# Performance work log

Hardware: AMD Instinct MI355X
Metric: run time of the kernel (lower is better)

## Reference

```python
import jax, jax.numpy as jnp
import numpy as np

SCALE = 256 ** -0.5  # d_proj ** -0.5

def setup_inputs() -> dict:
    key = jax.random.key(0)
    k1, k2, k3, k4 = jax.random.split(key, 4)
    B, L, T = 8, 2048, 512
    Dh, Dg, Dp = 1024, 768, 256
    H = jax.random.normal(k1, (B, L, Dh), dtype=jnp.float32)
    G = jax.random.normal(k2, (B, T, Dg), dtype=jnp.float32)
    mask = jnp.zeros((B, L), dtype=jnp.int32)  # True/nonzero = masked OUT
    Wk = jax.random.normal(k3, (Dh, Dp), dtype=jnp.float32) * (Dh ** -0.5)
    Wq = jax.random.normal(k4, (Dg, Dp), dtype=jnp.float32) * (Dg ** -0.5)
    return {"H": H, "G": G, "mask": mask, "Wk": Wk, "Wq": Wq}

def reference(H, G, mask, Wk, Wq):
    # K: [B,L,Dp], Q: [B,T,Dp]
    K = jnp.einsum('bld,dp->blp', H, Wk)
    Q = jnp.einsum('btd,dp->btp', G, Wq)
    # logits over keys L: [B,T,L]
    logits = jnp.einsum('btp,blp->btl', Q, K) * SCALE
    logits = jnp.where(mask[:, None, :] != 0, -jnp.inf, logits)
    alpha = jax.nn.softmax(logits, axis=-1)  # online-softmax in torch == exact softmax
    Z = jnp.einsum('btl,bld->btd', alpha, H)  # [B,T,Dh]
    return Z
```

## Files before the change

### kernel.cpp

```cpp
#include <hip/hip_runtime.h>
#include <math.h>

#define BATCH 8
#define LKEYS 2048
#define TQ    512
#define DH    1024
#define DG    768
#define DP    256
#define SCALE 0.0625f

typedef short  short8  __attribute__((ext_vector_type(8)));
typedef float  floatx4 __attribute__((ext_vector_type(4)));
typedef unsigned short u16x4 __attribute__((ext_vector_type(4)));
typedef unsigned short u16x8 __attribute__((ext_vector_type(8)));

typedef unsigned int __attribute__((address_space(1))) as1_uint;
typedef unsigned int __attribute__((address_space(3))) as3_uint;

__device__ __forceinline__ unsigned short f2b(float f) {
    union { float f; unsigned int u; } v; v.f = f;
    unsigned int u = v.u;
    unsigned int r = u + 0x7fffu + ((u >> 16) & 1u);
    if ((u & 0x7f800000u) == 0x7f800000u) r = u;
    return (unsigned short)(r >> 16);
}

__device__ __forceinline__ void gload_lds16(const void* g, void* l) {
    __builtin_amdgcn_global_load_lds((const as1_uint*)g, (as3_uint*)l, 16, 0, 0);
}

__host__ __device__ constexpr int wcnt_vm(int vm) {
    return (vm & 15) | (7 << 4) | (15 << 8);
}

template<int BM, int BN, int OMODE, int SWZ, int KSPLIT>
__global__ __launch_bounds__(256) void gemm_bf16_p(
    const unsigned short* __restrict__ Ap, const unsigned short* __restrict__ Bp,
    const int* __restrict__ maskp, void* __restrict__ Cp,
    int K, int lda, int ldb, int ldc,
    long sA, long sB, long sC, long sM, long sP, float scale)
{
    constexpr int FM = BM / 32, FN = BN / 32;
    constexpr int AI = BM / 64, BI = BN / 64;
    constexpr int NL = AI + BI;

    __shared__ unsigned short As[4][BM * 32];
    __shared__ unsigned short Bs[4][BN * 32];

    int bx = blockIdx.x, by = blockIdx.y, zz = blockIdx.z;
    if (SWZ == 1) {
        const int gx = gridDim.x;
        const int nwg = gx * gridDim.y;
        const int f = by * gx + bx;
        const int nper = nwg >> 3;
        const int fl = (f & 7) * nper + (f >> 3);
        bx = fl % gx; by = fl / gx;
    } else if (SWZ == 2) {
        const int gx = gridDim.x, nxy = gridDim.x * gridDim.y;
        const long l = blockIdx.x + (long)gx * (blockIdx.y + (long)gridDim.y * blockIdx.z);
        const int xcd  = (int)(l & 7);
        const int slot = (int)(l >> 3);
        zz = xcd + 8 * (slot / nxy);
        const int rem = slot % nxy;
        bx = rem % gx; by = rem / gx;
    }
    const int z    = (KSPLIT == 2) ? (zz & 7) : zz;
    const int half = (KSPLIT == 2) ? (zz >> 3) : 0;
    const int koff = half * K;

    const int tid  = threadIdx.x;
    const int lane = tid & 63;
    const int wid  = tid >> 6;
    const int wr   = wid >> 1, wc = wid & 1;
    const int lrow = lane & 15;
    const int g    = lane >> 4;

    const unsigned short* A = Ap + (long)z * sA + (long)(by * BM) * lda + koff;
    const unsigned short* B = Bp + (long)z * sB + (long)(bx * BN) * ldb + koff;
    const int srow = tid >> 2, sslot = tid & 3;

    const int nt = K / 32;
    floatx4 acc[FM][FN] = {};

    auto stage = [&](int t, int b) {
        const int k0 = t * 32;
        #pragma unroll
        for (int i = 0; i < AI; ++i)
            gload_lds16(A + (long)(srow + i * 64) * lda + k0 + sslot * 8,
                        (void*)&As[b][(i * 256 + tid) * 8]);
        #pragma unroll
        for (int i = 0; i < BI; ++i)
            gload_lds16(B + (long)(srow + i * 64) * ldb + k0 + sslot * 8,
                        (void*)&Bs[b][(i * 256 + tid) * 8]);
    };

    stage(0, 0);
    stage(1, 1);
    for (int t = 0; t < nt; ++t) {
        if (t + 2 < nt) {
            stage(t + 2, (t + 2) & 3);
            __builtin_amdgcn_s_waitcnt(wcnt_vm(2 * NL));
        } else if (t + 1 < nt) {
            __builtin_amdgcn_s_waitcnt(wcnt_vm(NL));
        } else {
            __builtin_amdgcn_s_waitcnt(wcnt_vm(0));
        }
        __builtin_amdgcn_s_barrier();
        __builtin_amdgcn_sched_barrier(0);

        const int b = t & 3;
        short8 a[FM], bf[FN];
        #pragma unroll
        for (int m = 0; m < FM; ++m)
            a[m] = *(const short8*)&As[b][(wr * (BM / 2) + m * 16 + lrow) * 32 + g * 8];
        #pragma unroll
        for (int n = 0; n < FN; ++n)
            bf[n] = *(const short8*)&Bs[b][(wc * (BN / 2) + n * 16 + lrow) * 32 + g * 8];
        __builtin_amdgcn_s_setprio(1);
        #pragma unroll
        for (int m = 0; m < FM; ++m)
            #pragma unroll
            for (int n = 0; n < FN; ++n)
                acc[m][n] = __builtin_amdgcn_mfma_f32_16x16x32_bf16(
                    a[m], bf[n], acc[m][n], 0, 0, 0);
        __builtin_amdgcn_s_setprio(0);
        __builtin_amdgcn_sched_barrier(0);
    }

    const int orow = by * BM + wr * (BM / 2);
    const int ocol = bx * BN + wc * (BN / 2);
    if (OMODE == 0) {
        float* C = (float*)Cp + (long)z * sC + (long)half * sP;
        #pragma unroll
        for (int m = 0; m < FM; ++m)
            #pragma unroll
            for (int n = 0; n < FN; ++n)
                #pragma unroll
                for (int r = 0; r < 4; ++r)
                    C[(long)(orow + m * 16 + 4 * g + r) * ldc + ocol + n * 16 + lrow]
                        = acc[m][n][r];
    } else if (OMODE == 1) {
        unsigned short* C = (unsigned short*)Cp + (long)z * sC;
        #pragma unroll
        for (int m = 0; m < FM; ++m)
            #pragma unroll
            for (int n = 0; n < FN; ++n)
                #pragma unroll
                for (int r = 0; r < 4; ++r)
                    C[(long)(orow + m * 16 + 4 * g + r) * ldc + ocol + n * 16 + lrow]
                        = f2b(acc[m][n][r]);
    } else {
        const int* mask = maskp + (long)z * sM;
        float* C = (float*)Cp + (long)z * sC;
        #pragma unroll
        for (int n = 0; n < FN; ++n) {
            int c = ocol + n * 16 + lrow;
            bool masked = (mask[c] != 0);
            #pragma unroll
            for (int m = 0; m < FM; ++m)
                #pragma unroll
                for (int r = 0; r < 4; ++r)
                    C[(long)(orow + m * 16 + 4 * g + r) * ldc + c]
                        = masked ? -INFINITY : acc[m][n][r] * scale;
        }
    }
}

__global__ __launch_bounds__(256) void reduce_add(
    const float4* __restrict__ P0, const float4* __restrict__ P1,
    float4* __restrict__ Zo)
{
    long i = (long)blockIdx.x * 256 + threadIdx.x;
    float4 a = P0[i], b = P1[i];
    Zo[i] = make_float4(a.x + b.x, a.y + b.y, a.z + b.z, a.w + b.w);
}

__global__ __launch_bounds__(256) void transpose_w(
    const float* __restrict__ W, unsigned short* __restrict__ WT, int D, int P)
{
    __shared__ float t[32][33];
    const int d0 = blockIdx.x * 32, p0 = blockIdx.y * 32;
    const int tx = threadIdx.x & 31, ty = threadIdx.x >> 5;
    #pragma unroll
    for (int j = 0; j < 4; ++j)
        t[ty + 8 * j][tx] = W[(long)(d0 + ty + 8 * j) * P + p0 + tx];
    __syncthreads();
    #pragma unroll
    for (int j = 0; j < 4; ++j)
        WT[(long)(p0 + ty + 8 * j) * D + d0 + tx] = f2b(t[tx][ty + 8 * j]);
}

__global__ __launch_bounds__(256) void prep_H(
    const float* __restrict__ H, unsigned short* __restrict__ Hb,
    unsigned short* __restrict__ HbT)
{
    __shared__ float tf[32][33];
    const int z = blockIdx.z;
    const int d0 = blockIdx.x * 32, l0 = blockIdx.y * 32;
    const float* Hz = H + (long)z * LKEYS * DH;
    unsigned short* Hbz = Hb + (long)z * LKEYS * DH;
    unsigned short* Tz = HbT + (long)z * DH * LKEYS;
    const int r = threadIdx.x >> 3, c = threadIdx.x & 7;
    float4 v = *(const float4*)&Hz[(long)(l0 + r) * DH + d0 + 4 * c];
    u16x4 w;
    w[0] = f2b(v.x); w[1] = f2b(v.y); w[2] = f2b(v.z); w[3] = f2b(v.w);
    *(u16x4*)&Hbz[(long)(l0 + r) * DH + d0 + 4 * c] = w;
    tf[r][4 * c + 0] = v.x; tf[r][4 * c + 1] = v.y;
    tf[r][4 * c + 2] = v.z; tf[r][4 * c + 3] = v.w;
    __syncthreads();
    u16x4 o;
    o[0] = f2b(tf[4 * c + 0][r]); o[1] = f2b(tf[4 * c + 1][r]);
    o[2] = f2b(tf[4 * c + 2][r]); o[3] = f2b(tf[4 * c + 3][r]);
    *(u16x4*)&Tz[(long)(d0 + r) * LKEYS + l0 + 4 * c] = o;
}

__global__ __launch_bounds__(256) void prep_G(
    const float* __restrict__ G, unsigned short* __restrict__ Gb)
{
    long i = ((long)blockIdx.x * 256 + threadIdx.x) * 8;
    float4 a = *(const float4*)&G[i];
    float4 b = *(const float4*)&G[i + 4];
    u16x8 w;
    w[0] = f2b(a.x); w[1] = f2b(a.y); w[2] = f2b(a.z); w[3] = f2b(a.w);
    w[4] = f2b(b.x); w[5] = f2b(b.y); w[6] = f2b(b.z); w[7] = f2b(b.w);
    *(u16x8*)&Gb[i] = w;
}

__global__ __launch_bounds__(256) void softmax_kernel(
    const float* __restrict__ S, unsigned short* __restrict__ Ab)
{
    const float4* row4 = (const float4*)(S + (long)blockIdx.x * LKEYS);
    u16x4* out4 = (u16x4*)(Ab + (long)blockIdx.x * LKEYS);
    const int tid = threadIdx.x;
    __shared__ float red[4];

    float4 v0 = row4[tid], v1 = row4[tid + 256];
    float m = fmaxf(fmaxf(fmaxf(v0.x, v0.y), fmaxf(v0.z, v0.w)),
                    fmaxf(fmaxf(v1.x, v1.y), fmaxf(v1.z, v1.w)));
    #pragma unroll
    for (int off = 32; off > 0; off >>= 1) m = fmaxf(m, __shfl_xor(m, off));
    if ((tid & 63) == 0) red[tid >> 6] = m;
    __syncthreads();
    m = fmaxf(fmaxf(red[0], red[1]), fmaxf(red[2], red[3]));

    float e[8];
    e[0] = __expf(v0.x - m); e[1] = __expf(v0.y - m);
    e[2] = __expf(v0.z - m); e[3] = __expf(v0.w - m);
    e[4] = __expf(v1.x - m); e[5] = __expf(v1.y - m);
    e[6] = __expf(v1.z - m); e[7] = __expf(v1.w - m);
    float s = ((e[0] + e[1]) + (e[2] + e[3])) + ((e[4] + e[5]) + (e[6] + e[7]));
    #pragma unroll
    for (int off = 32; off > 0; off >>= 1) s += __shfl_xor(s, off);
    __syncthreads();
    if ((tid & 63) == 0) red[tid >> 6] = s;
    __syncthreads();
    s = red[0] + red[1] + red[2] + red[3];

    float inv = 1.0f / s;
    u16x4 a0, a1;
    a0[0] = f2b(e[0] * inv); a0[1] = f2b(e[1] * inv);
    a0[2] = f2b(e[2] * inv); a0[3] = f2b(e[3] * inv);
    a1[0] = f2b(e[4] * inv); a1[1] = f2b(e[5] * inv);
    a1[2] = f2b(e[6] * inv); a1[3] = f2b(e[7] * inv);
    out4[tid] = a0; out4[tid + 256] = a1;
}

extern "C" void kernel_launch(void* const* d_in, const int* in_sizes, int n_in,
                              void* d_out, int out_size, void* d_ws, size_t ws_size,
                              hipStream_t stream)
{
    const float* H    = (const float*)d_in[0];
    const float* G    = (const float*)d_in[1];
    const int*   mask = (const int*)  d_in[2];
    const float* Wk   = (const float*)d_in[3];
    const float* Wq   = (const float*)d_in[4];
    float*       Z    = (float*)d_out;

    unsigned short* WkT = (unsigned short*)d_ws;
    unsigned short* WqT = WkT + 262144;
    unsigned short* Ab  = WqT + 196608;
    unsigned short* Kb  = Ab  + 8388608;
    unsigned short* Qb  = Kb  + 4194304;
    unsigned short* Gb  = Qb  + 1048576;
    unsigned short* HbT = Gb  + 3145728;
    unsigned short* Hb  = HbT + 16777216;
    float*          S   = (float*)Hb;
    float*          Zp  = (float*)Hb;

    transpose_w<<<dim3(DH / 32, DP / 32), 256, 0, stream>>>(Wk, WkT, DH, DP);
    transpose_w<<<dim3(DG / 32, DP / 32), 256, 0, stream>>>(Wq, WqT, DG, DP);

    prep_G<<<1536, 256, 0, stream>>>(G, Gb);
    prep_H<<<dim3(DH / 32, LKEYS / 32, BATCH), 256, 0, stream>>>(H, Hb, HbT);

    gemm_bf16_p<128, 64, 1, 1, 1><<<dim3(4, 128, 1), 256, 0, stream>>>(
        Hb, WkT, nullptr, Kb, DH, DH, DH, DP, 0, 0, 0, 0, 0, 1.f);

    gemm_bf16_p<64, 64, 1, 1, 1><<<dim3(4, 64, 1), 256, 0, stream>>>(
        Gb, WqT, nullptr, Qb, DG, DG, DG, DP, 0, 0, 0, 0, 0, 1.f);

    gemm_bf16_p<128, 128, 2, 2, 1><<<dim3(16, 4, BATCH), 256, 0, stream>>>(
        Qb, Kb, mask, S, DP, DP, DP, LKEYS,
        (long)TQ * DP, (long)LKEYS * DP, (long)TQ * LKEYS, (long)LKEYS, 0, SCALE);

    softmax_kernel<<<BATCH * TQ, 256, 0, stream>>>(S, Ab);

    gemm_bf16_p<128, 128, 0, 2, 2><<<dim3(8, 4, 2 * BATCH), 256, 0, stream>>>(
        Ab, HbT, nullptr, Zp, LKEYS / 2, LKEYS, LKEYS, DH,
        (long)TQ * LKEYS, (long)DH * LKEYS, (long)TQ * DH, 0,
        (long)BATCH * TQ * DH, 1.f);

    reduce_add<<<(BATCH * TQ * DH / 4) / 256, 256, 0, stream>>>(
        (const float4*)Zp, (const float4*)(Zp + (long)BATCH * TQ * DH),
        (float4*)Z);
}
```

Baseline: 121.2 us.

## Store logits and split-K partials in bf16, 4-way split-K with double buffering

Logits are now written by the QK^T GEMM as bf16 instead of fp32, and softmax reads the bf16 row. The final alpha·H GEMM is split four ways along K instead of two, writes bf16 partials and uses a new 2-buffer single-stage pipeline. A new reduce sums the four bf16 partials into fp32. The aim is to halve the memory traffic for the logits and partials and to give the final GEMM more parallelism. The cost is lost precision in the logits and partial sums, plus more partials to reduce.

After: 129.2 us. 6.6% more time.

```diff
diff --git a/kernel.cpp b/kernel.cpp
--- a/kernel.cpp
+++ b/kernel.cpp
@@ -24,6 +24,10 @@
     if ((u & 0x7f800000u) == 0x7f800000u) r = u;
     return (unsigned short)(r >> 16);
 }
+__device__ __forceinline__ float b2f(unsigned short b) {
+    union { unsigned int u; float f; } v; v.u = ((unsigned int)b) << 16;
+    return v.f;
+}
 
 __device__ __forceinline__ void gload_lds16(const void* g, void* l) {
     __builtin_amdgcn_global_load_lds((const as1_uint*)g, (as3_uint*)l, 16, 0, 0);
@@ -33,7 +37,7 @@
     return (vm & 15) | (7 << 4) | (15 << 8);
 }
 
-template<int BM, int BN, int OMODE, int SWZ, int KSPLIT>
+template<int BM, int BN, int OMODE, int SWZ, int KS, int PIPE>
 __global__ __launch_bounds__(256) void gemm_bf16_p(
     const unsigned short* __restrict__ Ap, const unsigned short* __restrict__ Bp,
     const int* __restrict__ maskp, void* __restrict__ Cp,
@@ -43,9 +47,10 @@
     constexpr int FM = BM / 32, FN = BN / 32;
     constexpr int AI = BM / 64, BI = BN / 64;
     constexpr int NL = AI + BI;
-
-    __shared__ unsigned short As[4][BM * 32];
-    __shared__ unsigned short Bs[4][BN * 32];
+    constexpr int NB = (PIPE == 1) ? 2 : 4;
+
+    __shared__ unsigned short As[NB][BM * 32];
+    __shared__ unsigned short Bs[NB][BN * 32];
 
     int bx = blockIdx.x, by = blockIdx.y, zz = blockIdx.z;
     if (SWZ == 1) {
@@ -64,9 +69,9 @@
         const int rem = slot % nxy;
         bx = rem % gx; by = rem / gx;
     }
-    const int z    = (KSPLIT == 2) ? (zz & 7) : zz;
-    const int half = (KSPLIT == 2) ? (zz >> 3) : 0;
-    const int koff = half * K;
+    const int z    = (KS > 1) ? (zz & 7) : zz;
+    const int part = (KS > 1) ? (zz >> 3) : 0;
+    const int koff = part * K;
 
     const int tid  = threadIdx.x;
     const int lane = tid & 63;
@@ -94,21 +99,7 @@
                         (void*)&Bs[b][(i * 256 + tid) * 8]);
     };
 
-    stage(0, 0);
-    stage(1, 1);
-    for (int t = 0; t < nt; ++t) {
-        if (t + 2 < nt) {
-            stage(t + 2, (t + 2) & 3);
-            __builtin_amdgcn_s_waitcnt(wcnt_vm(2 * NL));
-        } else if (t + 1 < nt) {
-            __builtin_amdgcn_s_waitcnt(wcnt_vm(NL));
-        } else {
-            __builtin_amdgcn_s_waitcnt(wcnt_vm(0));
-        }
-        __builtin_amdgcn_s_barrier();
-        __builtin_amdgcn_sched_barrier(0);
-
-        const int b = t & 3;
+    auto compute = [&](int b) {
         short8 a[FM], bf[FN];
         #pragma unroll
         for (int m = 0; m < FM; ++m)
@@ -125,12 +116,40 @@
                     a[m], bf[n], acc[m][n], 0, 0, 0);
         __builtin_amdgcn_s_setprio(0);
         __builtin_amdgcn_sched_barrier(0);
+    };
+
+    if (PIPE == 0) {
+        stage(0, 0);
+        stage(1, 1);
+        for (int t = 0; t < nt; ++t) {
+            if (t + 2 < nt) {
+                stage(t + 2, (t + 2) & 3);
+                __builtin_amdgcn_s_waitcnt(wcnt_vm(2 * NL));
+            } else if (t + 1 < nt) {
+                __builtin_amdgcn_s_waitcnt(wcnt_vm(NL));
+            } else {
+                __builtin_amdgcn_s_waitcnt(wcnt_vm(0));
+            }
+            __builtin_amdgcn_s_barrier();
+            __builtin_amdgcn_sched_barrier(0);
+            compute(t & 3);
+        }
+    } else {
+        stage(0, 0);
+        for (int t = 0; t < nt; ++t) {
+            __builtin_amdgcn_s_waitcnt(wcnt_vm(0));
+            __builtin_amdgcn_s_barrier();
+            __builtin_amdgcn_sched_barrier(0);
+            if (t + 1 < nt) stage(t + 1, (t + 1) & 1);
+            __builtin_amdgcn_sched_barrier(0);
+            compute(t & 1);
+        }
     }
 
     const int orow = by * BM + wr * (BM / 2);
     const int ocol = bx * BN + wc * (BN / 2);
     if (OMODE == 0) {
-        float* C = (float*)Cp + (long)z * sC + (long)half * sP;
+        float* C = (float*)Cp + (long)z * sC + (long)part * sP;
         #pragma unroll
         for (int m = 0; m < FM; ++m)
             #pragma unroll
@@ -140,7 +159,7 @@
                     C[(long)(orow + m * 16 + 4 * g + r) * ldc + ocol + n * 16 + lrow]
                         = acc[m][n][r];
     } else if (OMODE == 1) {
-        unsigned short* C = (unsigned short*)Cp + (long)z * sC;
+        unsigned short* C = (unsigned short*)Cp + (long)z * sC + (long)part * sP;
         #pragma unroll
         for (int m = 0; m < FM; ++m)
             #pragma unroll
@@ -149,7 +168,7 @@
                 for (int r = 0; r < 4; ++r)
                     C[(long)(orow + m * 16 + 4 * g + r) * ldc + ocol + n * 16 + lrow]
                         = f2b(acc[m][n][r]);
-    } else {
+    } else if (OMODE == 2) {
         const int* mask = maskp + (long)z * sM;
         float* C = (float*)Cp + (long)z * sC;
         #pragma unroll
@@ -163,16 +182,43 @@
                     C[(long)(orow + m * 16 + 4 * g + r) * ldc + c]
                         = masked ? -INFINITY : acc[m][n][r] * scale;
         }
+    } else {
+        const int* mask = maskp + (long)z * sM;
+        unsigned short* C = (unsigned short*)Cp + (long)z * sC;
+        #pragma unroll
+        for (int n = 0; n < FN; ++n) {
+            int c = ocol + n * 16 + lrow;
+            bool masked = (mask[c] != 0);
+            #pragma unroll
+            for (int m = 0; m < FM; ++m)
+                #pragma unroll
+                for (int r = 0; r < 4; ++r)
+                    C[(long)(orow + m * 16 + 4 * g + r) * ldc + c]
+                        = masked ? (unsigned short)0xFF80u
+                                 : f2b(acc[m][n][r] * scale);
+        }
     }
 }
 
-__global__ __launch_bounds__(256) void reduce_add(
-    const float4* __restrict__ P0, const float4* __restrict__ P1,
-    float4* __restrict__ Zo)
-{
-    long i = (long)blockIdx.x * 256 + threadIdx.x;
-    float4 a = P0[i], b = P1[i];
-    Zo[i] = make_float4(a.x + b.x, a.y + b.y, a.z + b.z, a.w + b.w);
+__global__ __launch_bounds__(256) void reduce_add4(
+    const unsigned short* __restrict__ P, long sP, float* __restrict__ Zo)
+{
+    long i = ((long)blockIdx.x * 256 + threadIdx.x) * 8;
+    u16x8 a = *(const u16x8*)&P[i];
+    u16x8 b = *(const u16x8*)&P[i + sP];
+    u16x8 c = *(const u16x8*)&P[i + 2 * sP];
+    u16x8 d = *(const u16x8*)&P[i + 3 * sP];
+    float4 o0, o1;
+    o0.x = (b2f(a[0]) + b2f(b[0])) + (b2f(c[0]) + b2f(d[0]));
+    o0.y = (b2f(a[1]) + b2f(b[1])) + (b2f(c[1]) + b2f(d[1]));
+    o0.z = (b2f(a[2]) + b2f(b[2])) + (b2f(c[2]) + b2f(d[2]));
+    o0.w = (b2f(a[3]) + b2f(b[3])) + (b2f(c[3]) + b2f(d[3]));
+    o1.x = (b2f(a[4]) + b2f(b[4])) + (b2f(c[4]) + b2f(d[4]));
+    o1.y = (b2f(a[5]) + b2f(b[5])) + (b2f(c[5]) + b2f(d[5]));
+    o1.z = (b2f(a[6]) + b2f(b[6])) + (b2f(c[6]) + b2f(d[6]));
+    o1.w = (b2f(a[7]) + b2f(b[7])) + (b2f(c[7]) + b2f(d[7]));
+    *(float4*)&Zo[i] = o0;
+    *(float4*)&Zo[i + 4] = o1;
 }
 
 __global__ __launch_bounds__(256) void transpose_w(
@@ -227,28 +273,29 @@
 }
 
 __global__ __launch_bounds__(256) void softmax_kernel(
-    const float* __restrict__ S, unsigned short* __restrict__ Ab)
-{
-    const float4* row4 = (const float4*)(S + (long)blockIdx.x * LKEYS);
-    u16x4* out4 = (u16x4*)(Ab + (long)blockIdx.x * LKEYS);
+    const unsigned short* __restrict__ S, unsigned short* __restrict__ Ab)
+{
+    const u16x8* row8 = (const u16x8*)(S + (long)blockIdx.x * LKEYS);
+    u16x8* out8 = (u16x8*)(Ab + (long)blockIdx.x * LKEYS);
     const int tid = threadIdx.x;
     __shared__ float red[4];
 
-    float4 v0 = row4[tid], v1 = row4[tid + 256];
-    float m = fmaxf(fmaxf(fmaxf(v0.x, v0.y), fmaxf(v0.z, v0.w)),
-                    fmaxf(fmaxf(v1.x, v1.y), fmaxf(v1.z, v1.w)));
+    u16x8 v = row8[tid];
+    float x[8];
+    #pragma unroll
+    for (int j = 0; j < 8; ++j) x[j] = b2f(v[j]);
+
+    float m = fmaxf(fmaxf(fmaxf(x[0], x[1]), fmaxf(x[2], x[3])),
+                    fmaxf(fmaxf(x[4], x[5]), fmaxf(x[6], x[7])));
     #pragma unroll
     for (int off = 32; off > 0; off >>= 1) m = fmaxf(m, __shfl_xor(m, off));
     if ((tid & 63) == 0) red[tid >> 6] = m;
     __syncthreads();
     m = fmaxf(fmaxf(red[0], red[1]), fmaxf(red[2], red[3]));
 
-    float e[8];
-    e[0] = __expf(v0.x - m); e[1] = __expf(v0.y - m);
-    e[2] = __expf(v0.z - m); e[3] = __expf(v0.w - m);
-    e[4] = __expf(v1.x - m); e[5] = __expf(v1.y - m);
-    e[6] = __expf(v1.z - m); e[7] = __expf(v1.w - m);
-    float s = ((e[0] + e[1]) + (e[2] + e[3])) + ((e[4] + e[5]) + (e[6] + e[7]));
+    float e[8], s = 0.f;
+    #pragma unroll
+    for (int j = 0; j < 8; ++j) { e[j] = __expf(x[j] - m); s += e[j]; }
     #pragma unroll
     for (int off = 32; off > 0; off >>= 1) s += __shfl_xor(s, off);
     __syncthreads();
@@ -257,12 +304,10 @@
     s = red[0] + red[1] + red[2] + red[3];
 
     float inv = 1.0f / s;
-    u16x4 a0, a1;
-    a0[0] = f2b(e[0] * inv); a0[1] = f2b(e[1] * inv);
-    a0[2] = f2b(e[2] * inv); a0[3] = f2b(e[3] * inv);
-    a1[0] = f2b(e[4] * inv); a1[1] = f2b(e[5] * inv);
-    a1[2] = f2b(e[6] * inv); a1[3] = f2b(e[7] * inv);
-    out4[tid] = a0; out4[tid + 256] = a1;
+    u16x8 o;
+    #pragma unroll
+    for (int j = 0; j < 8; ++j) o[j] = f2b(e[j] * inv);
+    out8[tid] = o;
 }
 
 extern "C" void kernel_launch(void* const* d_in, const int* in_sizes, int n_in,
@@ -284,8 +329,10 @@
     unsigned short* Gb  = Qb  + 1048576;
     unsigned short* HbT = Gb  + 3145728;
     unsigned short* Hb  = HbT + 16777216;
-    float*          S   = (float*)Hb;
-    float*          Zp  = (float*)Hb;
+    unsigned short* S   = Hb;
+    unsigned short* Zp  = Hb;
+    const long sZp = (long)BATCH * TQ * DH;
+    const long sZb = (long)TQ * DH;
 
     transpose_w<<<dim3(DH / 32, DP / 32), 256, 0, stream>>>(Wk, WkT, DH, DP);
     transpose_w<<<dim3(DG / 32, DP / 32), 256, 0, stream>>>(Wq, WqT, DG, DP);
@@ -293,24 +340,21 @@
     prep_G<<<1536, 256, 0, stream>>>(G, Gb);
     prep_H<<<dim3(DH / 32, LKEYS / 32, BATCH), 256, 0, stream>>>(H, Hb, HbT);
 
-    gemm_bf16_p<128, 64, 1, 1, 1><<<dim3(4, 128, 1), 256, 0, stream>>>(
+    gemm_bf16_p<128, 64, 1, 1, 1, 0><<<dim3(4, 128, 1), 256, 0, stream>>>(
         Hb, WkT, nullptr, Kb, DH, DH, DH, DP, 0, 0, 0, 0, 0, 1.f);
 
-    gemm_bf16_p<64, 64, 1, 1, 1><<<dim3(4, 64, 1), 256, 0, stream>>>(
+    gemm_bf16_p<64, 64, 1, 1, 1, 0><<<dim3(4, 64, 1), 256, 0, stream>>>(
         Gb, WqT, nullptr, Qb, DG, DG, DG, DP, 0, 0, 0, 0, 0, 1.f);
 
-    gemm_bf16_p<128, 128, 2, 2, 1><<<dim3(16, 4, BATCH), 256, 0, stream>>>(
+    gemm_bf16_p<128, 128, 3, 2, 1, 0><<<dim3(16, 4, BATCH), 256, 0, stream>>>(
         Qb, Kb, mask, S, DP, DP, DP, LKEYS,
         (long)TQ * DP, (long)LKEYS * DP, (long)TQ * LKEYS, (long)LKEYS, 0, SCALE);
 
     softmax_kernel<<<BATCH * TQ, 256, 0, stream>>>(S, Ab);
 
-    gemm_bf16_p<128, 128, 0, 2, 2><<<dim3(8, 4, 2 * BATCH), 256, 0, stream>>>(
-        Ab, HbT, nullptr, Zp, LKEYS / 2, LKEYS, LKEYS, DH,
-        (long)TQ * LKEYS, (long)DH * LKEYS, (long)TQ * DH, 0,
-        (long)BATCH * TQ * DH, 1.f);
-
-    reduce_add<<<(BATCH * TQ * DH / 4) / 256, 256, 0, stream>>>(
-        (const float4*)Zp, (const float4*)(Zp + (long)BATCH * TQ * DH),
-        (float4*)Z);
-}
+    gemm_bf16_p<128, 128, 1, 2, 4, 1><<<dim3(8, 4, 4 * BATCH), 256, 0, stream>>>(
+        Ab, HbT, nullptr, Zp, LKEYS / 4, LKEYS, LKEYS, DH,
+        (long)TQ * LKEYS, (long)DH * LKEYS, sZb, 0, sZp, 1.f);
+
+    reduce_add4<<<(int)(sZp / 8 / 256), 256, 0, stream>>>(Zp, sZp, Z);
+}
```
